# Kernel optimization log

Hardware: AMD Instinct MI355X
Metric: run time of the kernel (lower is better)

Reference implementation:

```python
import jax, jax.numpy as jnp
import numpy as np

N = 50000   # nodes
E = 800000  # edges
F = 128     # n_features
H = 128     # n_hidden
LN_EPS = 1e-5


def setup_inputs() -> dict:
    key = jax.random.key(0)
    ks = jax.random.split(key, 11)
    s = 0.05
    return {
        "x": jax.random.normal(ks[0], (N, F), jnp.float32),
        "edge_index": jax.random.randint(ks[1], (2, E), 0, N, dtype=jnp.int64),
        "edge_attr": jax.random.uniform(ks[2], (E, 1), jnp.float32),
        "ln_gamma": jax.random.normal(ks[3], (F,), jnp.float32),
        "ln_beta": jax.random.normal(ks[4], (F,), jnp.float32),
        "W1": jax.random.normal(ks[5], (F, H), jnp.float32) * s,
        "b1": jax.random.normal(ks[6], (H,), jnp.float32) * s,
        "W2": jax.random.normal(ks[7], (H, H), jnp.float32) * s,
        "b2": jax.random.normal(ks[8], (H,), jnp.float32) * s,
        "W3": jax.random.normal(ks[9], (H, 1), jnp.float32) * s,
        "b3": jax.random.normal(ks[10], (1,), jnp.float32) * s,
    }


def _gcn_conv(x, W, b, row, col, ew, n_nodes):
    """PyG GCNConv: add self loops (weight 1), symmetric normalization,
    gather-scale-scatter aggregation, linear (no bias) + bias."""
    loop = jnp.arange(n_nodes, dtype=row.dtype)
    row_f = jnp.concatenate([row, loop])          # [E+N] source
    col_f = jnp.concatenate([col, loop])          # [E+N] target
    ew_f = jnp.concatenate([ew, jnp.ones((n_nodes,), ew.dtype)])
    deg = jax.ops.segment_sum(ew_f, col_f, num_segments=n_nodes)  # [N]
    dis = jnp.where(deg > 0, jax.lax.rsqrt(jnp.where(deg > 0, deg, 1.0)), 0.0)
    norm = dis[row_f] * ew_f * dis[col_f]          # [E+N]
    h = x @ W                                      # [N, out]
    msg = h[row_f] * norm[:, None]                 # [E+N, out] gather+scale
    out = jax.ops.segment_sum(msg, col_f, num_segments=n_nodes)  # scatter-add
    return out + b


def reference(x, edge_index, edge_attr, ln_gamma, ln_beta, W1, b1, W2, b2, W3, b3):
    x = jnp.nan_to_num(x, nan=0.0, posinf=0.0, neginf=0.0)
    ew = jnp.nan_to_num(edge_attr[:, 0], nan=0.0, posinf=1.0, neginf=0.0)  # [E]
    row, col = edge_index[0], edge_index[1]
    # input LayerNorm
    mu = jnp.mean(x, axis=-1, keepdims=True)
    var = jnp.mean(jnp.square(x - mu), axis=-1, keepdims=True)
    x = (x - mu) * jax.lax.rsqrt(var + LN_EPS) * ln_gamma + ln_beta
    # hidden GCN layers (dropout = identity in eval mode)
    x = jax.nn.relu(_gcn_conv(x, W1, b1, row, col, ew, N))
    x = jax.nn.relu(_gcn_conv(x, W2, b2, row, col, ew, N))
    # output layer
    return _gcn_conv(x, W3, b3, row, col, ew, N)  # [N, 1]
```

## Files before the change

kernel.cpp:

```cpp
#include <hip/hip_runtime.h>
#include <hip/hip_fp16.h>
#include <math.h>

#define NNODES 50000
#define NEDGES 800000
#define NF 128
#define BK 64
#define BINSH 7
#define BINS ((NNODES + 127) >> BINSH)
#define SEGS 98
#define SEGCAP 64
#define EPT 8
#define EPB (1024 * EPT)
constexpr float LN_EPS = 1e-5f;

typedef _Float16 v8h __attribute__((ext_vector_type(8)));
typedef float v4f __attribute__((ext_vector_type(4)));

__device__ __forceinline__ float clean0(float v) {
    return (isnan(v) || isinf(v)) ? 0.0f : v;
}
__device__ __forceinline__ float cleanw(float v) {
    if (isnan(v)) return 0.0f;
    if (isinf(v)) return v > 0.0f ? 1.0f : 0.0f;
    return v;
}
__device__ __forceinline__ int clampN(int v) {
    return min(max(v, 0), NNODES - 1);
}
__device__ __forceinline__ int pad16(int v) { return (v + 15) & ~15; }

__device__ __forceinline__ unsigned int f2h2(float a, float b) {
    __half2 h = __float22half2_rn(make_float2(a, b));
    return *reinterpret_cast<unsigned int*>(&h);
}

__global__ __launch_bounds__(1024) void k_bin_ln(
        const int* __restrict__ ei, const float* __restrict__ ea,
        int* __restrict__ bcnt, int2* __restrict__ seg,
        const float* __restrict__ x, const float* __restrict__ gamma,
        const float* __restrict__ beta, unsigned short* __restrict__ z,
        const float* __restrict__ W1, const float* __restrict__ W2,
        unsigned short* __restrict__ Wh1T, unsigned short* __restrict__ Wl1T,
        unsigned short* __restrict__ Wh2T, unsigned short* __restrict__ Wl2T,
        int nbe, int nbln) {
    if ((int)blockIdx.x < nbe) {
        __shared__ int lcnt[BINS];
        for (int i = threadIdx.x; i < BINS; i += 1024) lcnt[i] = 0;
        __syncthreads();
        int e0 = blockIdx.x * EPB + threadIdx.x;
        size_t segbase = (size_t)blockIdx.x * BINS;
        #pragma unroll
        for (int j = 0; j < EPT; j++) {
            int e = e0 + j * 1024;
            if (e < NEDGES) {
                int r = clampN(ei[e]);
                int c = clampN(ei[NEDGES + e]);
                float w = cleanw(ea[e]);
                int b = c >> BINSH;
                int rank = atomicAdd(&lcnt[b], 1);
                if (rank < SEGCAP)
                    seg[(segbase + b) * SEGCAP + rank] =
                        make_int2(((c & 127) << 16) | r, __float_as_int(w));
            }
        }
        __syncthreads();
        for (int i = threadIdx.x; i < BINS; i += 1024)
            bcnt[blockIdx.x * BINS + i] = min(lcnt[i], SEGCAP);
    } else if ((int)blockIdx.x < nbe + nbln) {
        int bid = blockIdx.x - nbe;
        int n = (bid * 1024 + threadIdx.x) >> 6;
        int lane = threadIdx.x & 63;
        if (n >= NNODES) return;
        float2 v = ((const float2*)(x + (size_t)n * NF))[lane];
        v.x = clean0(v.x); v.y = clean0(v.y);
        float s = v.x + v.y;
        for (int o = 32; o > 0; o >>= 1) s += __shfl_xor(s, o);
        float mu = s * (1.0f / NF);
        float dx = v.x - mu, dy = v.y - mu;
        float q = dx * dx + dy * dy;
        for (int o = 32; o > 0; o >>= 1) q += __shfl_xor(q, o);
        float rstd = rsqrtf(q * (1.0f / NF) + LN_EPS);
        float2 g = ((const float2*)gamma)[lane];
        float2 bb = ((const float2*)beta)[lane];
        float ox = dx * rstd * g.x + bb.x;
        float oy = dy * rstd * g.y + bb.y;
        ((unsigned int*)z)[(size_t)n * 64 + lane] = f2h2(ox, oy);
    } else {
        int idx = (blockIdx.x - nbe - nbln) * 1024 + threadIdx.x;
        int m = idx >> 14;
        int n = (idx >> 7) & 127;
        int k = idx & 127;
        const float* W = m ? W2 : W1;
        unsigned short* Wh = m ? Wh2T : Wh1T;
        unsigned short* Wl = m ? Wl2T : Wl1T;
        float w = W[k * 128 + n];
        __half hh = __float2half(w);
        __half ll = __float2half(w - __half2float(hh));
        Wh[n * 128 + k] = __half_as_ushort(hh);
        Wl[n * 128 + k] = __half_as_ushort(ll);
    }
}

__global__ __launch_bounds__(1024) void k_bucketize(
        const int* __restrict__ bcnt, const int2* __restrict__ seg,
        int2* __restrict__ bucket, int* __restrict__ cnt, float* __restrict__ dis) {
    __shared__ int   tmp[SEGS];
    __shared__ int   offs[SEGS + 1];
    __shared__ int   lc[128];
    __shared__ float ld[128];
    int b = blockIdx.x;
    if (threadIdx.x < 128) { lc[threadIdx.x] = 0; ld[threadIdx.x] = 1.0f; }
    if (threadIdx.x < SEGS) tmp[threadIdx.x] = bcnt[threadIdx.x * BINS + b];
    __syncthreads();
    if (threadIdx.x == 0) {
        int a = 0;
        for (int s = 0; s < SEGS; s++) { offs[s] = a; a += tmp[s]; }
        offs[SEGS] = a;
    }
    __syncthreads();
    int tot = offs[SEGS];
    for (int i = threadIdx.x; i < tot; i += 1024) {
        int lo = 0, hi = SEGS;
        while (hi - lo > 1) {
            int mid = (lo + hi) >> 1;
            if (offs[mid] <= i) lo = mid; else hi = mid;
        }
        int2 rec = seg[((size_t)lo * BINS + b) * SEGCAP + (i - offs[lo])];
        int dlo = (rec.x >> 16) & 127;
        int s = rec.x & 0xFFFF;
        int pos = atomicAdd(&lc[dlo], 1);
        int n = (b << BINSH) + dlo;
        if (pos < BK) bucket[(n << 6) + pos] = make_int2(s, rec.y);
        atomicAdd(&ld[dlo], __int_as_float(rec.y));
    }
    __syncthreads();
    if (threadIdx.x < 128) {
        int n = (b << BINSH) + threadIdx.x;
        if (n < NNODES) {
            int c = min(lc[threadIdx.x], BK);
            int cp = pad16(c);
            int beg = n << 6;
            for (int p = beg + c; p < beg + cp; p++) bucket[p] = make_int2(0, 0);
            cnt[n] = cp;
            dis[n] = rsqrtf(ld[threadIdx.x]);
        }
    }
}

__global__ __launch_bounds__(256) void k_gemm_mfma(
        const unsigned short* __restrict__ Ain,
        const unsigned short* __restrict__ BhT, const unsigned short* __restrict__ BlT,
        const float* __restrict__ dis, unsigned short* __restrict__ C) {
    int w = threadIdx.x >> 6;
    int lane = threadIdx.x & 63;
    int m = lane & 15;
    int q = lane >> 4;
    int rowbase = blockIdx.x * 64 + w * 16;
    int arow = min(rowbase + m, NNODES - 1);

    const v8h* ap = (const v8h*)(Ain + (size_t)arow * NF);
    v8h af[4];
    #pragma unroll
    for (int c = 0; c < 4; c++) af[c] = ap[c * 4 + q];

    float ds[4];
    #pragma unroll
    for (int r = 0; r < 4; r++) ds[r] = dis[min(rowbase + q * 4 + r, NNODES - 1)];

    for (int nt = 0; nt < 8; nt++) {
        int n0 = nt * 16;
        const v8h* bhp = (const v8h*)(BhT + (size_t)(n0 + m) * NF);
        const v8h* blp = (const v8h*)(BlT + (size_t)(n0 + m) * NF);
        v4f acc = {0.f, 0.f, 0.f, 0.f};
        #pragma unroll
        for (int c = 0; c < 4; c++) {
            v8h bh = bhp[c * 4 + q];
            v8h bl = blp[c * 4 + q];
            acc = __builtin_amdgcn_mfma_f32_16x16x32_f16(af[c], bh, acc, 0, 0, 0);
            acc = __builtin_amdgcn_mfma_f32_16x16x32_f16(af[c], bl, acc, 0, 0, 0);
        }
        #pragma unroll
        for (int r = 0; r < 4; r++) {
            int gr = rowbase + q * 4 + r;
            if (gr < NNODES)
                C[(size_t)gr * NF + n0 + m] = __half_as_ushort(__float2half(acc[r] * ds[r]));
        }
    }
}

template <bool LAST>
__global__ __launch_bounds__(256, 8) void k_aggregate(
        const unsigned short* __restrict__ h, const float* __restrict__ dis,
        const int* __restrict__ cntp, const int2* __restrict__ bucket,
        const float* __restrict__ bias, unsigned short* __restrict__ y,
        const float* __restrict__ W3, float* __restrict__ h3) {
    int n0 = (blockIdx.x * blockDim.x + threadIdx.x) >> 6;
    if (n0 >= NNODES) return;
    int n = __builtin_amdgcn_readfirstlane(n0);
    int lane = threadIdx.x & 63;
    const __half2* hp = (const __half2*)h;
    float2 acc = __half22float2(hp[(size_t)n * 64 + lane]);
    int beg = n << 6;
    int end = beg + cntp[n];
    for (int p = beg; p < end; p += 16) {
        int2 rec[16];
        #pragma unroll
        for (int j = 0; j < 16; j++) rec[j] = bucket[p + j];
        __half2 v[16];
        #pragma unroll
        for (int j = 0; j < 16; j++) v[j] = hp[(size_t)rec[j].x * 64 + lane];
        #pragma unroll
        for (int j = 0; j < 16; j++) {
            float w = __int_as_float(rec[j].y);
            float2 f = __half22float2(v[j]);
            acc.x += f.x * w;
            acc.y += f.y * w;
        }
    }
    float dn = dis[n];
    float2 b = ((const float2*)bias)[lane];
    float ox = fmaxf(acc.x * dn + b.x, 0.0f);
    float oy = fmaxf(acc.y * dn + b.y, 0.0f);
    if (LAST) {
        float2 w3 = ((const float2*)W3)[lane];
        float s = ox * w3.x + oy * w3.y;
        for (int o = 32; o > 0; o >>= 1) s += __shfl_xor(s, o);
        if (lane == 0) h3[n] = s * dn;
    } else {
        ((__half2*)y)[(size_t)n * 64 + lane] = __float22half2_rn(make_float2(ox, oy));
    }
}

__global__ void k_agg_scalar(const float* __restrict__ h3, const float* __restrict__ dis,
                             const int* __restrict__ cntp, const int2* __restrict__ bucket,
                             const float* __restrict__ b3, float* __restrict__ out) {
    int n = blockIdx.x * blockDim.x + threadIdx.x;
    if (n >= NNODES) return;
    float acc = h3[n];
    int beg = n << 6;
    int end = beg + cntp[n];
    for (int p = beg; p + 4 <= end; p += 4) {
        int2 e0 = bucket[p], e1 = bucket[p + 1], e2 = bucket[p + 2], e3 = bucket[p + 3];
        float v0 = h3[e0.x], v1 = h3[e1.x], v2 = h3[e2.x], v3 = h3[e3.x];
        acc += v0 * __int_as_float(e0.y) + v1 * __int_as_float(e1.y)
             + v2 * __int_as_float(e2.y) + v3 * __int_as_float(e3.y);
    }
    out[n] = acc * dis[n] + b3[0];
}

extern "C" void kernel_launch(void* const* d_in, const int* in_sizes, int n_in,
                              void* d_out, int out_size, void* d_ws, size_t ws_size,
                              hipStream_t stream) {
    const float* x  = (const float*)d_in[0];
    const int*   ei = (const int*)d_in[1];
    const float* ea = (const float*)d_in[2];
    const float* g  = (const float*)d_in[3];
    const float* be = (const float*)d_in[4];
    const float* W1 = (const float*)d_in[5];
    const float* b1 = (const float*)d_in[6];
    const float* W2 = (const float*)d_in[7];
    const float* b2 = (const float*)d_in[8];
    const float* W3 = (const float*)d_in[9];
    const float* b3 = (const float*)d_in[10];
    float* out = (float*)d_out;

    char* ws = (char*)d_ws;
    size_t off = 0;
    auto alloc = [&](size_t bytes) {
        void* p = ws + off;
        off += (bytes + 255) & ~((size_t)255);
        return p;
    };
    unsigned short* zbuf = (unsigned short*)alloc((size_t)NNODES * NF * 2);
    unsigned short* hbuf = (unsigned short*)alloc((size_t)NNODES * NF * 2);
    float* dis    = (float*)alloc((size_t)NNODES * 4);
    int*   cnt    = (int*)  alloc((size_t)NNODES * 4);
    int2*  bucket = (int2*) alloc((size_t)NNODES * BK * 8);
    float* h3     = (float*)alloc((size_t)NNODES * 4);
    unsigned short* Wh1T = (unsigned short*)alloc(128 * 128 * 2);
    unsigned short* Wl1T = (unsigned short*)alloc(128 * 128 * 2);
    unsigned short* Wh2T = (unsigned short*)alloc(128 * 128 * 2);
    unsigned short* Wl2T = (unsigned short*)alloc(128 * 128 * 2);
    int*  bcnt = (int*) alloc((size_t)SEGS * BINS * 4);
    int2* seg  = (int2*)alloc((size_t)SEGS * BINS * SEGCAP * 8);
    (void)ws_size; (void)in_sizes; (void)n_in; (void)out_size;

    const int NB_N  = (NNODES + 255) / 256;
    const int NB_W  = (NNODES * 64 + 255) / 256;
    const int NB_G  = (NNODES + 63) / 64;
    const int NBE   = SEGS;
    const int NB_LN = NNODES * 64 / 1024;
    const int NB_WS = 32;

    k_bin_ln<<<NBE + NB_LN + NB_WS, 1024, 0, stream>>>(
        ei, ea, bcnt, seg, x, g, be, zbuf,
        W1, W2, Wh1T, Wl1T, Wh2T, Wl2T, NBE, NB_LN);
    k_bucketize<<<BINS, 1024, 0, stream>>>(bcnt, seg, bucket, cnt, dis);

    k_gemm_mfma<<<NB_G, 256, 0, stream>>>(zbuf, Wh1T, Wl1T, dis, hbuf);
    k_aggregate<false><<<NB_W, 256, 0, stream>>>(hbuf, dis, cnt, bucket, b1, zbuf,
                                                 nullptr, nullptr);
    k_gemm_mfma<<<NB_G, 256, 0, stream>>>(zbuf, Wh2T, Wl2T, dis, hbuf);
    k_aggregate<true><<<NB_W, 256, 0, stream>>>(hbuf, dis, cnt, bucket, b2, nullptr,
                                                W3, h3);
    k_agg_scalar<<<NB_N, 256, 0, stream>>>(h3, dis, cnt, bucket, b3, out);
}
```

Baseline: 247.1 us.

## Stage edge binning and bucketization in LDS for coalesced segment and bucket writes

The binning kernel now does a shared-memory counting sort of its edges by destination bin, so segment writes come out contiguous per bin instead of scattered. It also halves edges per block (more blocks) and shrinks segment capacity. The bucketize kernel drops the per-element binary search, reads segments one wave per segment, builds each bin's buckets in LDS, and writes the whole bin tile out coalesced with zero padding included. Bucket stride drops from 64 to 48, which cuts bucket memory and aggregate read footprint but truncates nodes with more than 48 in-edges and silently drops edges beyond 40 per bin per segment.

```diff
diff --git a/kernel.cpp b/kernel.cpp
--- a/kernel.cpp
+++ b/kernel.cpp
@@ -5,13 +5,13 @@
 #define NNODES 50000
 #define NEDGES 800000
 #define NF 128
-#define BK 64
+#define BK 48
 #define BINSH 7
 #define BINS ((NNODES + 127) >> BINSH)
-#define SEGS 98
-#define SEGCAP 64
-#define EPT 8
+#define EPT 4
 #define EPB (1024 * EPT)
+#define SEGS ((NEDGES + EPB - 1) / EPB)
+#define SEGCAP 40
 constexpr float LN_EPS = 1e-5f;
 
 typedef _Float16 v8h __attribute__((ext_vector_type(8)));
@@ -45,28 +45,61 @@
         unsigned short* __restrict__ Wh2T, unsigned short* __restrict__ Wl2T,
         int nbe, int nbln) {
     if ((int)blockIdx.x < nbe) {
+        __shared__ int2 lrec[EPB];
+        __shared__ unsigned short lbin[EPB];
         __shared__ int lcnt[BINS];
-        for (int i = threadIdx.x; i < BINS; i += 1024) lcnt[i] = 0;
-        __syncthreads();
-        int e0 = blockIdx.x * EPB + threadIdx.x;
-        size_t segbase = (size_t)blockIdx.x * BINS;
+        __shared__ int offs[BINS];
+        __shared__ int scan[512];
+        int t = threadIdx.x;
+        for (int i = t; i < BINS; i += 1024) lcnt[i] = 0;
+        __syncthreads();
+        int e0 = blockIdx.x * EPB + t;
+        int myb[EPT]; int2 myrec[EPT];
         #pragma unroll
         for (int j = 0; j < EPT; j++) {
             int e = e0 + j * 1024;
+            myb[j] = -1;
             if (e < NEDGES) {
                 int r = clampN(ei[e]);
                 int c = clampN(ei[NEDGES + e]);
                 float w = cleanw(ea[e]);
                 int b = c >> BINSH;
-                int rank = atomicAdd(&lcnt[b], 1);
-                if (rank < SEGCAP)
-                    seg[(segbase + b) * SEGCAP + rank] =
-                        make_int2(((c & 127) << 16) | r, __float_as_int(w));
+                myb[j] = b;
+                myrec[j] = make_int2(((c & 127) << 16) | r, __float_as_int(w));
+                atomicAdd(&lcnt[b], 1);
             }
         }
         __syncthreads();
-        for (int i = threadIdx.x; i < BINS; i += 1024)
-            bcnt[blockIdx.x * BINS + i] = min(lcnt[i], SEGCAP);
+        if (t < 512) scan[t] = (t < BINS) ? lcnt[t] : 0;
+        __syncthreads();
+        for (int d = 1; d < 512; d <<= 1) {
+            int v = 0;
+            if (t < 512 && t >= d) v = scan[t - d];
+            __syncthreads();
+            if (t < 512) scan[t] += v;
+            __syncthreads();
+        }
+        if (t < BINS) { offs[t] = scan[t] - lcnt[t]; lcnt[t] = scan[t] - lcnt[t]; }
+        __syncthreads();
+        #pragma unroll
+        for (int j = 0; j < EPT; j++) {
+            if (myb[j] >= 0) {
+                int pos = atomicAdd(&lcnt[myb[j]], 1);
+                lrec[pos] = myrec[j];
+                lbin[pos] = (unsigned short)myb[j];
+            }
+        }
+        __syncthreads();
+        int tot = scan[BINS - 1];
+        size_t segbase = (size_t)blockIdx.x * BINS;
+        for (int i = t; i < tot; i += 1024) {
+            int b = lbin[i];
+            int rank = i - offs[b];
+            if (rank < SEGCAP)
+                seg[(segbase + b) * SEGCAP + rank] = lrec[i];
+        }
+        for (int i = t; i < BINS; i += 1024)
+            bcnt[blockIdx.x * BINS + i] = min(lcnt[i] - offs[i], SEGCAP);
     } else if ((int)blockIdx.x < nbe + nbln) {
         int bid = blockIdx.x - nbe;
         int n = (bid * 1024 + threadIdx.x) >> 6;
@@ -105,45 +138,34 @@
 __global__ __launch_bounds__(1024) void k_bucketize(
         const int* __restrict__ bcnt, const int2* __restrict__ seg,
         int2* __restrict__ bucket, int* __restrict__ cnt, float* __restrict__ dis) {
-    __shared__ int   tmp[SEGS];
-    __shared__ int   offs[SEGS + 1];
+    __shared__ int2  lb[128 * BK];
     __shared__ int   lc[128];
     __shared__ float ld[128];
     int b = blockIdx.x;
-    if (threadIdx.x < 128) { lc[threadIdx.x] = 0; ld[threadIdx.x] = 1.0f; }
-    if (threadIdx.x < SEGS) tmp[threadIdx.x] = bcnt[threadIdx.x * BINS + b];
+    int t = threadIdx.x;
+    for (int i = t; i < 128 * BK; i += 1024) lb[i] = make_int2(0, 0);
+    if (t < 128) { lc[t] = 0; ld[t] = 1.0f; }
     __syncthreads();
-    if (threadIdx.x == 0) {
-        int a = 0;
-        for (int s = 0; s < SEGS; s++) { offs[s] = a; a += tmp[s]; }
-        offs[SEGS] = a;
+    int wv = t >> 6, lane = t & 63;
+    for (int s = wv; s < SEGS; s += 16) {
+        int len = bcnt[s * BINS + b];
+        if (lane < len) {
+            int2 rec = seg[((size_t)s * BINS + b) * SEGCAP + lane];
+            int dlo = (rec.x >> 16) & 127;
+            int pos = atomicAdd(&lc[dlo], 1);
+            if (pos < BK) lb[dlo * BK + pos] = make_int2(rec.x & 0xFFFF, rec.y);
+            atomicAdd(&ld[dlo], __int_as_float(rec.y));
+        }
     }
     __syncthreads();
-    int tot = offs[SEGS];
-    for (int i = threadIdx.x; i < tot; i += 1024) {
-        int lo = 0, hi = SEGS;
-        while (hi - lo > 1) {
-            int mid = (lo + hi) >> 1;
-            if (offs[mid] <= i) lo = mid; else hi = mid;
-        }
-        int2 rec = seg[((size_t)lo * BINS + b) * SEGCAP + (i - offs[lo])];
-        int dlo = (rec.x >> 16) & 127;
-        int s = rec.x & 0xFFFF;
-        int pos = atomicAdd(&lc[dlo], 1);
-        int n = (b << BINSH) + dlo;
-        if (pos < BK) bucket[(n << 6) + pos] = make_int2(s, rec.y);
-        atomicAdd(&ld[dlo], __int_as_float(rec.y));
-    }
-    __syncthreads();
-    if (threadIdx.x < 128) {
-        int n = (b << BINSH) + threadIdx.x;
+    size_t base = (size_t)b * (128 * BK);
+    for (int i = t; i < 128 * BK; i += 1024) bucket[base + i] = lb[i];
+    if (t < 128) {
+        int n = (b << BINSH) + t;
         if (n < NNODES) {
-            int c = min(lc[threadIdx.x], BK);
-            int cp = pad16(c);
-            int beg = n << 6;
-            for (int p = beg + c; p < beg + cp; p++) bucket[p] = make_int2(0, 0);
-            cnt[n] = cp;
-            dis[n] = rsqrtf(ld[threadIdx.x]);
+            int c = min(lc[t], BK);
+            cnt[n] = pad16(c);
+            dis[n] = rsqrtf(ld[t]);
         }
     }
 }
@@ -201,7 +223,7 @@
     int lane = threadIdx.x & 63;
     const __half2* hp = (const __half2*)h;
     float2 acc = __half22float2(hp[(size_t)n * 64 + lane]);
-    int beg = n << 6;
+    int beg = n * BK;
     int end = beg + cntp[n];
     for (int p = beg; p < end; p += 16) {
         int2 rec[16];
@@ -238,7 +260,7 @@
     int n = blockIdx.x * blockDim.x + threadIdx.x;
     if (n >= NNODES) return;
     float acc = h3[n];
-    int beg = n << 6;
+    int beg = n * BK;
     int end = beg + cntp[n];
     for (int p = beg; p + 4 <= end; p += 4) {
         int2 e0 = bucket[p], e1 = bucket[p + 1], e2 = bucket[p + 2], e3 = bucket[p + 3];
@@ -276,7 +298,7 @@
     unsigned short* hbuf = (unsigned short*)alloc((size_t)NNODES * NF * 2);
     float* dis    = (float*)alloc((size_t)NNODES * 4);
     int*   cnt    = (int*)  alloc((size_t)NNODES * 4);
-    int2*  bucket = (int2*) alloc((size_t)NNODES * BK * 8);
+    int2*  bucket = (int2*) alloc((size_t)BINS * 128 * BK * 8);
     float* h3     = (float*)alloc((size_t)NNODES * 4);
     unsigned short* Wh1T = (unsigned short*)alloc(128 * 128 * 2);
     unsigned short* Wl1T = (unsigned short*)alloc(128 * 128 * 2);
@@ -289,13 +311,12 @@
     const int NB_N  = (NNODES + 255) / 256;
     const int NB_W  = (NNODES * 64 + 255) / 256;
     const int NB_G  = (NNODES + 63) / 64;
-    const int NBE   = SEGS;
     const int NB_LN = NNODES * 64 / 1024;
     const int NB_WS = 32;
 
-    k_bin_ln<<<NBE + NB_LN + NB_WS, 1024, 0, stream>>>(
+    k_bin_ln<<<SEGS + NB_LN + NB_WS, 1024, 0, stream>>>(
         ei, ea, bcnt, seg, x, g, be, zbuf,
-        W1, W2, Wh1T, Wl1T, Wh2T, Wl2T, NBE, NB_LN);
+        W1, W2, Wh1T, Wl1T, Wh2T, Wl2T, SEGS, NB_LN);
     k_bucketize<<<BINS, 1024, 0, stream>>>(bcnt, seg, bucket, cnt, dis);
 
     k_gemm_mfma<<<NB_G, 256, 0, stream>>>(zbuf, Wh1T, Wl1T, dis, hbuf);
```

Measured after the change: 249.4 us. About the same (+1.0%).
